# Kernel optimization log

Measured on AMD Instinct MI355X. Metric: run time of the kernel, lower is better.

The kernel has to match this reference:

```python
import jax, jax.numpy as jnp
import numpy as np

N = 100000
E = 640000
ND = 128   # node_dim
ED = 128   # edge_dim
HD = 256   # hidden_dim
EPS = 1e-5


def _mlp_ln(x, W1, b1, W2, b2, W3, b3, g, beta):
    h = jax.nn.relu(x @ W1 + b1)
    h = jax.nn.relu(h @ W2 + b2)
    o = h @ W3 + b3
    mu = jnp.mean(o, axis=-1, keepdims=True)
    var = jnp.mean(jnp.square(o - mu), axis=-1, keepdims=True)
    return (o - mu) * jax.lax.rsqrt(var + EPS) * g + beta


def setup_inputs() -> dict:
    key = jax.random.key(0)
    ks = jax.random.split(key, 20)
    s = 0.02
    inp = {
        "node_emb": jax.random.normal(ks[0], (N, ND), jnp.float32),
        "edge_emb": jax.random.normal(ks[1], (E, ED), jnp.float32),
        "src": jax.random.randint(ks[2], (E,), 0, N),
        "dst": jax.random.randint(ks[3], (E,), 0, N),
        "num_nodes": N,
        # edge MLP: in = 2*ND + ED
        "eW1": jax.random.normal(ks[4], (2 * ND + ED, HD), jnp.float32) * s,
        "eb1": jnp.zeros((HD,), jnp.float32),
        "eW2": jax.random.normal(ks[5], (HD, HD), jnp.float32) * s,
        "eb2": jnp.zeros((HD,), jnp.float32),
        "eW3": jax.random.normal(ks[6], (HD, ED), jnp.float32) * s,
        "eb3": jnp.zeros((ED,), jnp.float32),
        "eg": jnp.ones((ED,), jnp.float32),
        "ebeta": jnp.zeros((ED,), jnp.float32),
        # node MLP: in = ND + ED
        "nW1": jax.random.normal(ks[7], (ND + ED, HD), jnp.float32) * s,
        "nb1": jnp.zeros((HD,), jnp.float32),
        "nW2": jax.random.normal(ks[8], (HD, HD), jnp.float32) * s,
        "nb2": jnp.zeros((HD,), jnp.float32),
        "nW3": jax.random.normal(ks[9], (HD, ND), jnp.float32) * s,
        "nb3": jnp.zeros((ND,), jnp.float32),
        "ng": jnp.ones((ND,), jnp.float32),
        "nbeta": jnp.zeros((ND,), jnp.float32),
    }
    return inp


def reference(node_emb, edge_emb, src, dst, num_nodes,
              eW1, eb1, eW2, eb2, eW3, eb3, eg, ebeta,
              nW1, nb1, nW2, nb2, nW3, nb3, ng, nbeta):
    # Edge update: e' = MLP(concat(h_i, h_j, e)) + e
    edge_input = jnp.concatenate([node_emb[src], node_emb[dst], edge_emb], axis=-1)
    edge_emb_new = _mlp_ln(edge_input, eW1, eb1, eW2, eb2, eW3, eb3, eg, ebeta) + edge_emb
    # Mean aggregation over incoming edges per dst node
    agg = jax.ops.segment_sum(edge_emb_new, dst, num_segments=num_nodes)
    count = jax.ops.segment_sum(jnp.ones((dst.shape[0], 1), node_emb.dtype), dst, num_segments=num_nodes)
    agg = agg / jnp.maximum(count, 1.0)
    # Node update: h' = MLP(concat(h, agg)) + h
    node_input = jnp.concatenate([node_emb, agg], axis=-1)
    node_emb_new = _mlp_ln(node_input, nW1, nb1, nW2, nb2, nW3, nb3, ng, nbeta) + node_emb
    return (node_emb_new, edge_emb_new)
```

## Files before the change

kernel.cpp:

```cpp
#include <hip/hip_runtime.h>
#include <hip/hip_bf16.h>

typedef __attribute__((ext_vector_type(8))) short bf16x8;
typedef __attribute__((ext_vector_type(4))) float f32x4;

__device__ __forceinline__ short f2bf(float f) {
  union { __hip_bfloat16 h; short s; } u;
  u.h = __float2bfloat16(f);
  return u.s;
}

__device__ __forceinline__ void gld_lds16(const short* g, short* l) {
  __builtin_amdgcn_global_load_lds((const __attribute__((address_space(1))) unsigned*)g,
                                   (__attribute__((address_space(3))) unsigned*)l,
                                   16, 0, 0);
}

template <int NSLOTS>
__device__ __forceinline__ void stage(const short* __restrict__ g, short* l, int tid) {
#pragma unroll
  for (int s0 = 0; s0 < NSLOTS / 256; ++s0) {
    int s = s0 * 256 + tid;
    gld_lds16(g + (size_t)s * 8, l + (size_t)s * 8);
  }
}

__global__ void prep_kernel(const float* __restrict__ W, short* __restrict__ out, int K, int N) {
  int s = blockIdx.x * 256 + threadIdx.x;
  int NF = N >> 4;
  int total = (K >> 5) * NF * 64;
  if (s >= total) return;
  int l = s & 63, kcf = s >> 6;
  int kc = kcf / NF, f = kcf - kc * NF;
  int kg = l >> 4, l16 = l & 15;
  const float* p = W + (size_t)(kc * 32 + kg * 8) * N + f * 16 + l16;
  bf16x8 o;
#pragma unroll
  for (int e = 0; e < 8; ++e) o[e] = f2bf(p[(size_t)e * N]);
  *(bf16x8*)(out + (size_t)s * 8) = o;
}

__global__ void count_kernel(const int* __restrict__ dst, int* __restrict__ cnt, int E) {
  int i = blockIdx.x * 256 + threadIdx.x;
  if (i < E) atomicAdd(&cnt[dst[i]], 1);
}

__global__ __launch_bounds__(1024) void scan_kernel(const int* __restrict__ cnt,
                                                    int* __restrict__ off,
                                                    int* __restrict__ cursor, int N) {
  __shared__ int wsum[16];
  const int t = threadIdx.x;
  const int w = t >> 6, l = t & 63;
  int running = 0;
  for (int base = 0; base < N; base += 1024) {
    int i = base + t;
    int v = (i < N) ? cnt[i] : 0;
    int x = v;
#pragma unroll
    for (int d = 1; d < 64; d <<= 1) { int y = __shfl_up(x, d); if (l >= d) x += y; }
    if (l == 63) wsum[w] = x;
    __syncthreads();
    if (w == 0) {
      int s = (l < 16) ? wsum[l] : 0;
#pragma unroll
      for (int d = 1; d < 16; d <<= 1) { int y = __shfl_up(s, d); if (l >= d) s += y; }
      if (l < 16) wsum[l] = s;
    }
    __syncthreads();
    int total = wsum[15];
    int wo = (w > 0) ? wsum[w - 1] : 0;
    int excl = running + wo + x - v;
    if (i < N) { off[i] = excl; cursor[i] = excl; }
    running += total;
    __syncthreads();
  }
  if (t == 0) off[N] = running;
}

__global__ void scatter_kernel(const int* __restrict__ dst, int* __restrict__ cursor,
                               int* __restrict__ eidx, int E) {
  int e = blockIdx.x * 256 + threadIdx.x;
  if (e < E) {
    int p = atomicAdd(&cursor[dst[e]], 1);
    eidx[p] = e;
  }
}

__global__ void agg_kernel(const float* __restrict__ edge_out, const int* __restrict__ eidx,
                           const int* __restrict__ off, float* __restrict__ agg, int N) {
  int n = blockIdx.x * 4 + (threadIdx.x >> 6);
  if (n >= N) return;
  int l = threadIdx.x & 63;
  int beg = off[n], end = off[n + 1];
  float ax = 0.f, ay = 0.f;
  int i = beg;
  for (; i + 4 <= end; i += 4) {
    int e0 = eidx[i], e1 = eidx[i + 1], e2 = eidx[i + 2], e3 = eidx[i + 3];
    float2 v0 = *(const float2*)(edge_out + (size_t)e0 * 128 + l * 2);
    float2 v1 = *(const float2*)(edge_out + (size_t)e1 * 128 + l * 2);
    float2 v2 = *(const float2*)(edge_out + (size_t)e2 * 128 + l * 2);
    float2 v3 = *(const float2*)(edge_out + (size_t)e3 * 128 + l * 2);
    ax += v0.x + v1.x + v2.x + v3.x;
    ay += v0.y + v1.y + v2.y + v3.y;
  }
  for (; i < end; ++i) {
    int e = eidx[i];
    float2 v = *(const float2*)(edge_out + (size_t)e * 128 + l * 2);
    ax += v.x; ay += v.y;
  }
  float inv = 1.0f / fmaxf((float)(end - beg), 1.0f);
  *(float2*)(agg + (size_t)n * 128 + l * 2) = make_float2(ax * inv, ay * inv);
}

struct F8 { float4 a, b; };

template <bool IS_EDGE>
__launch_bounds__(256, 2)
__global__ void mlp_kernel(const float* __restrict__ node_emb, const float* __restrict__ edge_emb,
                           const int* __restrict__ src, const int* __restrict__ dst,
                           const short* __restrict__ w1p, const short* __restrict__ w2p,
                           const short* __restrict__ w3p,
                           const float* __restrict__ b1, const float* __restrict__ b2,
                           const float* __restrict__ b3,
                           const float* __restrict__ gam, const float* __restrict__ bet,
                           const float* __restrict__ agg,
                           float* __restrict__ out_base, int M) {
  __shared__ short Bs[2][8192];
  __shared__ short Hs[16384];

  const int tid = threadIdx.x;
  const int bid = blockIdx.x;
  const int m0 = bid * 64;
  const int w = tid >> 6, lane = tid & 63, l16 = lane & 15, kg = lane >> 4;

  constexpr int NC1 = IS_EDGE ? 12 : 8;
  const int r1 = bid % NC1;
  const int r2 = bid & 7;
  auto c1 = [&](int i) { int c = r1 + i; return c < NC1 ? c : c - NC1; };
  auto c2 = [&](int i) { return (r2 + i) & 7; };

  const int grow = tid >> 2;
  const int gco = (tid & 3) * 8;
  const int grc = min(m0 + grow, M - 1);
  const int aslot = (grow >> 4) * 64 + (tid & 3) * 16 + (grow & 15);
  int gsr = 0, gdr = 0;
  if (IS_EDGE) { gsr = src[grc]; gdr = dst[grc]; }

  float b1v[4], b2v[4];
#pragma unroll
  for (int ct = 0; ct < 4; ++ct) {
    int col = w * 64 + ct * 16 + l16;
    b1v[ct] = b1[col];
    b2v[ct] = b2[col];
  }
  float b3v[8], gv[8], bev[8];
#pragma unroll
  for (int f = 0; f < 8; ++f) {
    int col = f * 16 + l16;
    b3v[f] = b3[col]; gv[f] = gam[col]; bev[f] = bet[col];
  }

  f32x4 acc[16];
#pragma unroll
  for (int i = 0; i < 16; ++i) { f32x4 z = {0.f, 0.f, 0.f, 0.f}; acc[i] = z; }

  auto gatherA = [&](int c) -> F8 {
    const float* q;
    if (IS_EDGE) {
      if (c < 4)      q = node_emb + (size_t)gsr * 128 + c * 32 + gco;
      else if (c < 8) q = node_emb + (size_t)gdr * 128 + (c - 4) * 32 + gco;
      else            q = edge_emb + (size_t)grc * 128 + (c - 8) * 32 + gco;
    } else {
      if (c < 4)      q = node_emb + (size_t)grc * 128 + c * 32 + gco;
      else            q = agg + (size_t)grc * 128 + (c - 4) * 32 + gco;
    }
    F8 r;
    r.a = *(const float4*)q;
    r.b = *(const float4*)(q + 4);
    return r;
  };
  auto writeA = [&](const F8& p, int buf) {
    float tmp[8];
    *(float4*)tmp = p.a; *(float4*)(tmp + 4) = p.b;
    bf16x8 o;
#pragma unroll
    for (int e = 0; e < 8; ++e) o[e] = f2bf(tmp[e]);
    *(bf16x8*)&Hs[(size_t)(buf * 256 + aslot) * 8] = o;
  };
  auto compNS = [&](const short* Abase, const short* Bbase) {
    bf16x8 a[4], b[4];
#pragma unroll
    for (int rt = 0; rt < 4; ++rt) a[rt] = *(const bf16x8*)&Abase[(size_t)(rt * 64 + kg * 16 + l16) * 8];
#pragma unroll
    for (int ct = 0; ct < 4; ++ct) b[ct] = *(const bf16x8*)&Bbase[(size_t)((w * 4 + ct) * 64 + lane) * 8];
#pragma unroll
    for (int rt = 0; rt < 4; ++rt)
#pragma unroll
      for (int ct = 0; ct < 4; ++ct)
        acc[rt * 4 + ct] = __builtin_amdgcn_mfma_f32_16x16x32_bf16(a[rt], b[ct], acc[rt * 4 + ct], 0, 0, 0);
  };
  auto compH = [&](int kc, const short* Bbase) {
    bf16x8 a[4], b[4];
#pragma unroll
    for (int rt = 0; rt < 4; ++rt) {
      int row = rt * 16 + l16, cg = kc * 4 + kg;
      a[rt] = *(const bf16x8*)&Hs[(size_t)(row * 32 + (cg ^ (row & 7))) * 8];
    }
#pragma unroll
    for (int ct = 0; ct < 4; ++ct) b[ct] = *(const bf16x8*)&Bbase[(size_t)((w * 4 + ct) * 64 + lane) * 8];
#pragma unroll
    for (int rt = 0; rt < 4; ++rt)
#pragma unroll
      for (int ct = 0; ct < 4; ++ct)
        acc[rt * 4 + ct] = __builtin_amdgcn_mfma_f32_16x16x32_bf16(a[rt], b[ct], acc[rt * 4 + ct], 0, 0, 0);
  };
  auto writeH = [&](const float* bias4) {
#pragma unroll
    for (int ct = 0; ct < 4; ++ct) {
      int col = w * 64 + ct * 16 + l16;
      int cg = col >> 3, el = col & 7;
      float bv = bias4[ct];
#pragma unroll
      for (int rt = 0; rt < 4; ++rt) {
        f32x4 v = acc[rt * 4 + ct];
#pragma unroll
        for (int q = 0; q < 4; ++q) {
          int row = rt * 16 + kg * 4 + q;
          Hs[(size_t)(row * 32 + (cg ^ (row & 7))) * 8 + el] = f2bf(fmaxf(v[q] + bv, 0.f));
        }
        f32x4 z = {0.f, 0.f, 0.f, 0.f};
        acc[rt * 4 + ct] = z;
      }
    }
  };

  F8 p0 = gatherA(c1(0));
  stage<1024>(w1p + (size_t)c1(0) * 8192, Bs[0], tid);
  F8 sHold = gatherA(c1(1));
  writeA(p0, 0);
  __syncthreads();

  int curB = 0, curA = 0;
#pragma unroll
  for (int i = 0; i < NC1; ++i) {
    const short* nxt = (i + 1 < NC1) ? w1p + (size_t)c1(i + 1) * 8192
                                     : w2p + (size_t)c2(0) * 8192;
    stage<1024>(nxt, Bs[curB ^ 1], tid);
    __builtin_amdgcn_sched_barrier(0);
    F8 pin = sHold;
    if (i + 2 < NC1) pin = gatherA(c1(i + 2));
    __builtin_amdgcn_sched_barrier(0);
    compNS(&Hs[(size_t)curA * 2048], Bs[curB]);
    if (i + 1 < NC1) writeA(sHold, curA ^ 1);
    if (i + 2 < NC1) asm volatile("s_waitcnt vmcnt(2) lgkmcnt(0)" ::: "memory");
    else             asm volatile("s_waitcnt vmcnt(0) lgkmcnt(0)" ::: "memory");
    __builtin_amdgcn_s_barrier();
    __builtin_amdgcn_sched_barrier(0);
    curB ^= 1;
    if (i + 1 < NC1) curA ^= 1;
    sHold = pin;
  }
  writeH(b1v);
  __syncthreads();

#pragma unroll
  for (int j = 0; j < 8; ++j) {
    if (j < 7) stage<1024>(w2p + (size_t)c2(j + 1) * 8192, Bs[curB ^ 1], tid);
    else       stage<512>(w3p + (size_t)c2(0) * 4096, Bs[curB ^ 1], tid);
    compH(c2(j), Bs[curB]);
    __syncthreads();
    curB ^= 1;
  }
  writeH(b2v);
  __syncthreads();

#pragma unroll
  for (int j = 0; j < 8; ++j) {
    if (j < 7) stage<512>(w3p + (size_t)c2(j + 1) * 4096, Bs[curB ^ 1], tid);
    {
      int row = w * 16 + l16, cg = c2(j) * 4 + kg;
      bf16x8 a = *(const bf16x8*)&Hs[(size_t)(row * 32 + (cg ^ (row & 7))) * 8];
#pragma unroll
      for (int f = 0; f < 8; ++f) {
        bf16x8 b = *(const bf16x8*)&Bs[curB][(size_t)(f * 64 + lane) * 8];
        acc[f] = __builtin_amdgcn_mfma_f32_16x16x32_bf16(a, b, acc[f], 0, 0, 0);
      }
    }
    if (j < 7) { __syncthreads(); curB ^= 1; }
  }

#pragma unroll
  for (int q = 0; q < 4; ++q) {
    int rg = m0 + w * 16 + kg * 4 + q;
    float o[8], s1 = 0.f, s2 = 0.f;
#pragma unroll
    for (int f = 0; f < 8; ++f) {
      float x = acc[f][q] + b3v[f];
      o[f] = x; s1 += x; s2 += x * x;
    }
#pragma unroll
    for (int m = 1; m <= 8; m <<= 1) { s1 += __shfl_xor(s1, m); s2 += __shfl_xor(s2, m); }
    float mu = s1 * (1.f / 128.f);
    float var = s2 * (1.f / 128.f) - mu * mu;
    float rs = rsqrtf(var + 1e-5f);
    if (rg < M) {
      const float* resid = (IS_EDGE ? edge_emb : node_emb) + (size_t)rg * 128;
      float* op = out_base + (size_t)rg * 128;
#pragma unroll
      for (int f = 0; f < 8; ++f) {
        int col = f * 16 + l16;
        op[col] = (o[f] - mu) * rs * gv[f] + bev[f] + resid[col];
      }
    }
  }
}

extern "C" void kernel_launch(void* const* d_in, const int* in_sizes, int n_in,
                              void* d_out, int out_size, void* d_ws, size_t ws_size,
                              hipStream_t stream) {
  const float* node_emb = (const float*)d_in[0];
  const float* edge_emb = (const float*)d_in[1];
  const int*   src      = (const int*)d_in[2];
  const int*   dst      = (const int*)d_in[3];
  const float* eW1 = (const float*)d_in[5];
  const float* eb1 = (const float*)d_in[6];
  const float* eW2 = (const float*)d_in[7];
  const float* eb2 = (const float*)d_in[8];
  const float* eW3 = (const float*)d_in[9];
  const float* eb3 = (const float*)d_in[10];
  const float* eg  = (const float*)d_in[11];
  const float* ebt = (const float*)d_in[12];
  const float* nW1 = (const float*)d_in[13];
  const float* nb1 = (const float*)d_in[14];
  const float* nW2 = (const float*)d_in[15];
  const float* nb2 = (const float*)d_in[16];
  const float* nW3 = (const float*)d_in[17];
  const float* nb3 = (const float*)d_in[18];
  const float* ng  = (const float*)d_in[19];
  const float* nbt = (const float*)d_in[20];

  const int Nn = in_sizes[0] / 128;
  const int Ee = in_sizes[2];

  char* ws = (char*)d_ws;
  float* agg  = (float*)ws;  ws += (size_t)Nn * 128 * 4;
  int* cnt_i  = (int*)ws;    ws += (size_t)Nn * 4;
  int* cursor = (int*)ws;    ws += (size_t)Nn * 4;
  int* offv   = (int*)ws;    ws += (size_t)(Nn + 1) * 4;
  int* eidx   = (int*)ws;    ws += (size_t)Ee * 4;
  ws = (char*)(((uintptr_t)ws + 15) & ~(uintptr_t)15);
  short* wp = (short*)ws;
  short* eW1p = wp;
  short* eW2p = wp + 98304;
  short* eW3p = wp + 163840;
  short* nW1p = wp + 196608;
  short* nW2p = wp + 262144;
  short* nW3p = wp + 327680;

  float* out_node = (float*)d_out;
  float* out_edge = out_node + (size_t)Nn * 128;

  hipMemsetAsync(cnt_i, 0, (size_t)Nn * 4, stream);

  prep_kernel<<<48, 256, 0, stream>>>(eW1, eW1p, 384, 256);
  prep_kernel<<<32, 256, 0, stream>>>(eW2, eW2p, 256, 256);
  prep_kernel<<<16, 256, 0, stream>>>(eW3, eW3p, 256, 128);
  prep_kernel<<<32, 256, 0, stream>>>(nW1, nW1p, 256, 256);
  prep_kernel<<<32, 256, 0, stream>>>(nW2, nW2p, 256, 256);
  prep_kernel<<<16, 256, 0, stream>>>(nW3, nW3p, 256, 128);

  count_kernel<<<(Ee + 255) / 256, 256, 0, stream>>>(dst, cnt_i, Ee);
  scan_kernel<<<1, 1024, 0, stream>>>(cnt_i, offv, cursor, Nn);
  scatter_kernel<<<(Ee + 255) / 256, 256, 0, stream>>>(dst, cursor, eidx, Ee);

  mlp_kernel<true><<<(Ee + 63) / 64, 256, 0, stream>>>(
      node_emb, edge_emb, src, dst, eW1p, eW2p, eW3p,
      eb1, eb2, eb3, eg, ebt, agg, out_edge, Ee);

  agg_kernel<<<(Nn + 3) / 4, 256, 0, stream>>>(out_edge, eidx, offv, agg, Nn);

  mlp_kernel<false><<<(Nn + 63) / 64, 256, 0, stream>>>(
      node_emb, edge_emb, src, dst, nW1p, nW2p, nW3p,
      nb1, nb2, nb3, ng, nbt, agg, out_node, Nn);
}
```

Before: 817.3 us.

## Use 128-row tiles with 512 threads and triple-buffered contiguous weight stream

The fused MLP kernel now processes 128 rows per block with 8 waves arranged 2x4. Each staged weight chunk is therefore reused across twice as many rows, which halves weight traffic into LDS per output row. All three layer weights are packed into one contiguous buffer and streamed through a 3-slot LDS ring using global-to-LDS loads. The hidden activations use a new swizzled row-major layout, and the matching K permutation is applied in prep_kernel for W2 and W3. The kernel needs 128 KB of dynamic LDS per block, which limits each CU to one block and ties correctness to the permuted weight layout matching the writeH and read swizzles.

```diff
diff --git a/kernel.cpp b/kernel.cpp
--- a/kernel.cpp
+++ b/kernel.cpp
@@ -2,6 +2,7 @@
 #include <hip/hip_bf16.h>
 
 typedef __attribute__((ext_vector_type(8))) short bf16x8;
+typedef __attribute__((ext_vector_type(4))) short s16x4;
 typedef __attribute__((ext_vector_type(4))) float f32x4;
 
 __device__ __forceinline__ short f2bf(float f) {
@@ -16,15 +17,10 @@
                                    16, 0, 0);
 }
 
-template <int NSLOTS>
-__device__ __forceinline__ void stage(const short* __restrict__ g, short* l, int tid) {
-#pragma unroll
-  for (int s0 = 0; s0 < NSLOTS / 256; ++s0) {
-    int s = s0 * 256 + tid;
-    gld_lds16(g + (size_t)s * 8, l + (size_t)s * 8);
-  }
-}
-
+#define BARX(N) asm volatile("s_waitcnt vmcnt(" #N ") lgkmcnt(0)\ns_barrier" ::: "memory")
+#define BARLG() asm volatile("s_waitcnt lgkmcnt(0)\ns_barrier" ::: "memory")
+
+template <bool PERM>
 __global__ void prep_kernel(const float* __restrict__ W, short* __restrict__ out, int K, int N) {
   int s = blockIdx.x * 256 + threadIdx.x;
   int NF = N >> 4;
@@ -33,10 +29,13 @@
   int l = s & 63, kcf = s >> 6;
   int kc = kcf / NF, f = kcf - kc * NF;
   int kg = l >> 4, l16 = l & 15;
-  const float* p = W + (size_t)(kc * 32 + kg * 8) * N + f * 16 + l16;
   bf16x8 o;
 #pragma unroll
-  for (int e = 0; e < 8; ++e) o[e] = f2bf(p[(size_t)e * N]);
+  for (int e = 0; e < 8; ++e) {
+    int kh = kc * 32 + kg * 8 + e;
+    int k = PERM ? ((kh & ~63) | ((kh & 3) << 4) | ((kh >> 2) & 15)) : kh;
+    o[e] = f2bf(W[(size_t)k * N + f * 16 + l16]);
+  }
   *(bf16x8*)(out + (size_t)s * 8) = o;
 }
 
@@ -115,41 +114,38 @@
 struct F8 { float4 a, b; };
 
 template <bool IS_EDGE>
-__launch_bounds__(256, 2)
+__launch_bounds__(512, 2)
 __global__ void mlp_kernel(const float* __restrict__ node_emb, const float* __restrict__ edge_emb,
                            const int* __restrict__ src, const int* __restrict__ dst,
-                           const short* __restrict__ w1p, const short* __restrict__ w2p,
-                           const short* __restrict__ w3p,
+                           const short* __restrict__ wAll,
                            const float* __restrict__ b1, const float* __restrict__ b2,
                            const float* __restrict__ b3,
                            const float* __restrict__ gam, const float* __restrict__ bet,
                            const float* __restrict__ agg,
                            float* __restrict__ out_base, int M) {
-  __shared__ short Bs[2][8192];
-  __shared__ short Hs[16384];
+  extern __shared__ short smem[];
+  short* BsBase = smem;
+  short* AsBase = smem + 24576;
+  short* Hs     = smem + 32768;
 
   const int tid = threadIdx.x;
-  const int bid = blockIdx.x;
-  const int m0 = bid * 64;
+  const int m0 = blockIdx.x * 128;
   const int w = tid >> 6, lane = tid & 63, l16 = lane & 15, kg = lane >> 4;
+  const int wr = w >> 2, wc = w & 3;
 
   constexpr int NC1 = IS_EDGE ? 12 : 8;
-  const int r1 = bid % NC1;
-  const int r2 = bid & 7;
-  auto c1 = [&](int i) { int c = r1 + i; return c < NC1 ? c : c - NC1; };
-  auto c2 = [&](int i) { return (r2 + i) & 7; };
 
   const int grow = tid >> 2;
-  const int gco = (tid & 3) * 8;
+  const int gk = tid & 3;
   const int grc = min(m0 + grow, M - 1);
-  const int aslot = (grow >> 4) * 64 + (tid & 3) * 16 + (grow & 15);
+  const int aslot = (grow >> 4) * 64 + gk * 16 + (grow & 15);
   int gsr = 0, gdr = 0;
   if (IS_EDGE) { gsr = src[grc]; gdr = dst[grc]; }
 
   float b1v[4], b2v[4];
 #pragma unroll
   for (int ct = 0; ct < 4; ++ct) {
-    int col = w * 64 + ct * 16 + l16;
+    int col = wc * 64 + ct * 16 + l16;
     b1v[ct] = b1[col];
     b2v[ct] = b2[col];
   }
@@ -164,15 +160,23 @@
 #pragma unroll
   for (int i = 0; i < 16; ++i) { f32x4 z = {0.f, 0.f, 0.f, 0.f}; acc[i] = z; }
 
+  auto bsbuf = [&](int v) -> short* { return BsBase + (size_t)(v % 3) * 8192; };
+  auto stage1024 = [&](int v) {
+    const short* g = wAll + (size_t)v * 8192;
+    short* l = bsbuf(v);
+    gld_lds16(g + (size_t)tid * 8, l + (size_t)tid * 8);
+    gld_lds16(g + (size_t)(512 + tid) * 8, l + (size_t)(512 + tid) * 8);
+  };
+
   auto gatherA = [&](int c) -> F8 {
     const float* q;
     if (IS_EDGE) {
-      if (c < 4)      q = node_emb + (size_t)gsr * 128 + c * 32 + gco;
-      else if (c < 8) q = node_emb + (size_t)gdr * 128 + (c - 4) * 32 + gco;
-      else            q = edge_emb + (size_t)grc * 128 + (c - 8) * 32 + gco;
+      if (c < 4)      q = node_emb + (size_t)gsr * 128 + c * 32 + gk * 8;
+      else if (c < 8) q = node_emb + (size_t)gdr * 128 + (c - 4) * 32 + gk * 8;
+      else            q = edge_emb + (size_t)grc * 128 + (c - 8) * 32 + gk * 8;
     } else {
-      if (c < 4)      q = node_emb + (size_t)grc * 128 + c * 32 + gco;
-      else            q = agg + (size_t)grc * 128 + (c - 4) * 32 + gco;
+      if (c < 4) q = node_emb + (size_t)grc * 128 + c * 32 + gk * 8;
+      else       q = agg + (size_t)grc * 128 + (c - 4) * 32 + gk * 8;
     }
     F8 r;
     r.a = *(const float4*)q;
@@ -180,113 +184,116 @@
     return r;
   };
   auto writeA = [&](const F8& p, int buf) {
-    float tmp[8];
-    *(float4*)tmp = p.a; *(float4*)(tmp + 4) = p.b;
+    float t[8];
+    *(float4*)t = p.a; *(float4*)(t + 4) = p.b;
     bf16x8 o;
 #pragma unroll
-    for (int e = 0; e < 8; ++e) o[e] = f2bf(tmp[e]);
-    *(bf16x8*)&Hs[(size_t)(buf * 256 + aslot) * 8] = o;
-  };
-  auto compNS = [&](const short* Abase, const short* Bbase) {
-    bf16x8 a[4], b[4];
-#pragma unroll
-    for (int rt = 0; rt < 4; ++rt) a[rt] = *(const bf16x8*)&Abase[(size_t)(rt * 64 + kg * 16 + l16) * 8];
-#pragma unroll
-    for (int ct = 0; ct < 4; ++ct) b[ct] = *(const bf16x8*)&Bbase[(size_t)((w * 4 + ct) * 64 + lane) * 8];
+    for (int e = 0; e < 8; ++e) o[e] = f2bf(t[e]);
+    *(bf16x8*)&AsBase[(size_t)buf * 4096 + (size_t)aslot * 8] = o;
+  };
+
+  auto mfma16 = [&](bf16x8* a, bf16x8* b) {
 #pragma unroll
     for (int rt = 0; rt < 4; ++rt)
 #pragma unroll
       for (int ct = 0; ct < 4; ++ct)
         acc[rt * 4 + ct] = __builtin_amdgcn_mfma_f32_16x16x32_bf16(a[rt], b[ct], acc[rt * 4 + ct], 0, 0, 0);
   };
-  auto compH = [&](int kc, const short* Bbase) {
+
+  auto compA = [&](int i) {
+    const short* Ap = AsBase + (size_t)(i & 1) * 4096;
+    const short* Bp = bsbuf(i);
     bf16x8 a[4], b[4];
 #pragma unroll
+    for (int rt = 0; rt < 4; ++rt)
+      a[rt] = *(const bf16x8*)&Ap[(size_t)((wr * 4 + rt) * 64 + kg * 16 + l16) * 8];
+#pragma unroll
+    for (int ct = 0; ct < 4; ++ct)
+      b[ct] = *(const bf16x8*)&Bp[(size_t)((wc * 4 + ct) * 64 + lane) * 8];
+    mfma16(a, b);
+  };
+
+  auto computeH = [&](int j, const short* Bp) {
+    bf16x8 a[4], b[4];
+#pragma unroll
     for (int rt = 0; rt < 4; ++rt) {
-      int row = rt * 16 + l16, cg = kc * 4 + kg;
-      a[rt] = *(const bf16x8*)&Hs[(size_t)(row * 32 + (cg ^ (row & 7))) * 8];
-    }
-#pragma unroll
-    for (int ct = 0; ct < 4; ++ct) b[ct] = *(const bf16x8*)&Bbase[(size_t)((w * 4 + ct) * 64 + lane) * 8];
+      int row = wr * 64 + rt * 16 + l16;
+      int ch = (j * 32 + kg * 8) ^ ((row & 7) << 3);
+      a[rt] = *(const bf16x8*)&Hs[(size_t)row * 256 + ch];
+    }
+#pragma unroll
+    for (int ct = 0; ct < 4; ++ct)
+      b[ct] = *(const bf16x8*)&Bp[(size_t)((wc * 4 + ct) * 64 + lane) * 8];
+    mfma16(a, b);
+  };
+
+  auto writeH = [&](const float* bv) {
 #pragma unroll
     for (int rt = 0; rt < 4; ++rt)
 #pragma unroll
-      for (int ct = 0; ct < 4; ++ct)
-        acc[rt * 4 + ct] = __builtin_amdgcn_mfma_f32_16x16x32_bf16(a[rt], b[ct], acc[rt * 4 + ct], 0, 0, 0);
-  };
-  auto writeH = [&](const float* bias4) {
-#pragma unroll
-    for (int ct = 0; ct < 4; ++ct) {
-      int col = w * 64 + ct * 16 + l16;
-      int cg = col >> 3, el = col & 7;
-      float bv = bias4[ct];
-#pragma unroll
-      for (int rt = 0; rt < 4; ++rt) {
-        f32x4 v = acc[rt * 4 + ct];
-#pragma unroll
-        for (int q = 0; q < 4; ++q) {
-          int row = rt * 16 + kg * 4 + q;
-          Hs[(size_t)(row * 32 + (cg ^ (row & 7))) * 8 + el] = f2bf(fmaxf(v[q] + bv, 0.f));
-        }
-        f32x4 z = {0.f, 0.f, 0.f, 0.f};
-        acc[rt * 4 + ct] = z;
+      for (int q = 0; q < 4; ++q) {
+        int row = wr * 64 + rt * 16 + kg * 4 + q;
+        s16x4 v;
+#pragma unroll
+        for (int ct = 0; ct < 4; ++ct)
+          v[ct] = f2bf(fmaxf(acc[rt * 4 + ct][q] + bv[ct], 0.f));
+        int ch = (wc * 64 + l16 * 4) ^ ((row & 7) << 3);
+        *(s16x4*)&Hs[(size_t)row * 256 + ch] = v;
       }
-    }
-  };
-
-  F8 p0 = gatherA(c1(0));
-  stage<1024>(w1p + (size_t)c1(0) * 8192, Bs[0], tid);
-  F8 sHold = gatherA(c1(1));
-  writeA(p0, 0);
-  __syncthreads();
-
-  int curB = 0, curA = 0;
+#pragma unroll
+    for (int i = 0; i < 16; ++i) { f32x4 z = {0.f, 0.f, 0.f, 0.f}; acc[i] = z; }
+  };
+
+  auto computeL3 = [&](int kk, const short* Bp) {
+    int row = w * 16 + l16;
+    int ch = (kk * 32 + kg * 8) ^ ((row & 7) << 3);
+    bf16x8 a = *(const bf16x8*)&Hs[(size_t)row * 256 + ch];
+    const short* Bsub = Bp + (size_t)(kk & 1) * 4096;
+#pragma unroll
+    for (int f = 0; f < 8; ++f) {
+      bf16x8 b = *(const bf16x8*)&Bsub[(size_t)(f * 64 + lane) * 8];
+      acc[f] = __builtin_amdgcn_mfma_f32_16x16x32_bf16(a, b, acc[f], 0, 0, 0);
+    }
+  };
+
+  F8 hold0 = gatherA(0);
+  stage1024(0);
+  stage1024(1);
+  F8 hold = gatherA(1);
+  writeA(hold0, 0);
+  BARX(4);
+
 #pragma unroll
   for (int i = 0; i < NC1; ++i) {
-    const short* nxt = (i + 1 < NC1) ? w1p + (size_t)c1(i + 1) * 8192
-                                     : w2p + (size_t)c2(0) * 8192;
-    stage<1024>(nxt, Bs[curB ^ 1], tid);
-    __builtin_amdgcn_sched_barrier(0);
-    F8 pin = sHold;
-    if (i + 2 < NC1) pin = gatherA(c1(i + 2));
-    __builtin_amdgcn_sched_barrier(0);
-    compNS(&Hs[(size_t)curA * 2048], Bs[curB]);
-    if (i + 1 < NC1) writeA(sHold, curA ^ 1);
-    if (i + 2 < NC1) asm volatile("s_waitcnt vmcnt(2) lgkmcnt(0)" ::: "memory");
-    else             asm volatile("s_waitcnt vmcnt(0) lgkmcnt(0)" ::: "memory");
-    __builtin_amdgcn_s_barrier();
-    __builtin_amdgcn_sched_barrier(0);
-    curB ^= 1;
-    if (i + 1 < NC1) curA ^= 1;
-    sHold = pin;
+    stage1024(i + 2);
+    F8 gnew = hold;
+    if (i + 2 < NC1) gnew = gatherA(i + 2);
+    compA(i);
+    if (i + 1 < NC1) writeA(hold, (i + 1) & 1);
+    if (i + 2 < NC1) { BARX(4); } else { BARX(2); }
+    hold = gnew;
   }
   writeH(b1v);
-  __syncthreads();
+  BARLG();
 
 #pragma unroll
   for (int j = 0; j < 8; ++j) {
-    if (j < 7) stage<1024>(w2p + (size_t)c2(j + 1) * 8192, Bs[curB ^ 1], tid);
-    else       stage<512>(w3p + (size_t)c2(0) * 4096, Bs[curB ^ 1], tid);
-    compH(c2(j), Bs[curB]);
-    __syncthreads();
-    curB ^= 1;
+    int p = NC1 + j;
+    stage1024(p + 2);
+    computeH(j, bsbuf(p));
+    BARX(2);
   }
   writeH(b2v);
-  __syncthreads();
-
-#pragma unroll
-  for (int j = 0; j < 8; ++j) {
-    if (j < 7) stage<512>(w3p + (size_t)c2(j + 1) * 4096, Bs[curB ^ 1], tid);
-    {
-      int row = w * 16 + l16, cg = c2(j) * 4 + kg;
-      bf16x8 a = *(const bf16x8*)&Hs[(size_t)(row * 32 + (cg ^ (row & 7))) * 8];
-#pragma unroll
-      for (int f = 0; f < 8; ++f) {
-        bf16x8 b = *(const bf16x8*)&Bs[curB][(size_t)(f * 64 + lane) * 8];
-        acc[f] = __builtin_amdgcn_mfma_f32_16x16x32_bf16(a, b, acc[f], 0, 0, 0);
-      }
-    }
-    if (j < 7) { __syncthreads(); curB ^= 1; }
+  BARLG();
+
+#pragma unroll
+  for (int k = 0; k < 4; ++k) {
+    int p = NC1 + 8 + k;
+    if (k < 2) stage1024(p + 2);
+    computeL3(2 * k, bsbuf(p));
+    computeL3(2 * k + 1, bsbuf(p));
+    if (k == 0 || k == 1) { BARX(2); }
+    else if (k == 2)      { BARX(0); }
   }
 
 #pragma unroll
@@ -350,36 +357,32 @@
   int* eidx   = (int*)ws;    ws += (size_t)Ee * 4;
   ws = (char*)(((uintptr_t)ws + 15) & ~(uintptr_t)15);
   short* wp = (short*)ws;
-  short* eW1p = wp;
-  short* eW2p = wp + 98304;
-  short* eW3p = wp + 163840;
-  short* nW1p = wp + 196608;
-  short* nW2p = wp + 262144;
-  short* nW3p = wp + 327680;
+  short* eAll = wp;
+  short* nAll = wp + 196608;
 
   float* out_node = (float*)d_out;
   float* out_edge = out_node + (size_t)Nn * 128;
 
   hipMemsetAsync(cnt_i, 0, (size_t)Nn * 4, stream);
 
-  prep_kernel<<<48, 256, 0, stream>>>(eW1, eW1p, 384, 256);
-  prep_kernel<<<32, 256, 0, stream>>>(eW2, eW2p, 256, 256);
-  prep_kernel<<<16, 256, 0, stream>>>(eW3, eW3p, 256, 128);
-  prep_kernel<<<32, 256, 0, stream>>>(nW1, nW1p, 256, 256);
-  prep_kernel<<<32, 256, 0, stream>>>(nW2, nW2p, 256, 256);
-  prep_kernel<<<16, 256, 0, stream>>>(nW3, nW3p, 256, 128);
+  prep_kernel<false><<<48, 256, 0, stream>>>(eW1, eAll, 384, 256);
+  prep_kernel<true><<<32, 256, 0, stream>>>(eW2, eAll + 98304, 256, 256);
+  prep_kernel<true><<<16, 256, 0, stream>>>(eW3, eAll + 163840, 256, 128);
+  prep_kernel<false><<<32, 256, 0, stream>>>(nW1, nAll, 256, 256);
+  prep_kernel<true><<<32, 256, 0, stream>>>(nW2, nAll + 65536, 256, 256);
+  prep_kernel<true><<<16, 256, 0, stream>>>(nW3, nAll + 131072, 256, 128);
 
   count_kernel<<<(Ee + 255) / 256, 256, 0, stream>>>(dst, cnt_i, Ee);
   scan_kernel<<<1, 1024, 0, stream>>>(cnt_i, offv, cursor, Nn);
   scatter_kernel<<<(Ee + 255) / 256, 256, 0, stream>>>(dst, cursor, eidx, Ee);
 
-  mlp_kernel<true><<<(Ee + 63) / 64, 256, 0, stream>>>(
-      node_emb, edge_emb, src, dst, eW1p, eW2p, eW3p,
+  mlp_kernel<true><<<(Ee + 127) / 128, 512, 131072, stream>>>(
+      node_emb, edge_emb, src, dst, eAll,
       eb1, eb2, eb3, eg, ebt, agg, out_edge, Ee);
 
   agg_kernel<<<(Nn + 3) / 4, 256, 0, stream>>>(out_edge, eidx, offv, agg, Nn);
 
-  mlp_kernel<false><<<(Nn + 63) / 64, 256, 0, stream>>>(
-      node_emb, edge_emb, src, dst, nW1p, nW2p, nW3p,
+  mlp_kernel<false><<<(Nn + 127) / 128, 512, 131072, stream>>>(
+      node_emb, edge_emb, src, dst, nAll,
       nb1, nb2, nb3, ng, nbt, agg, out_node, Nn);
 }
```

Result: faster. 751.8 us (-8.0%).
